# Kernel tuning notes

Hardware: AMD Instinct MI355X
Metric: run time of the kernel (lower is better)

Reference implementation:

```python
import jax, jax.numpy as jnp
import numpy as np

# Fixed architecture constants (from source / MambaConfig)
B_ = 8          # batch
L_ = 2048       # seq_len
D_MODEL = 6     # input_size / d_model
ED = 48         # expand_factor * d_model = hidden_size
N = 32          # d_state
DCONV = 16      # d_conv
NLAYERS = 4
DTRANK = 1      # ceil(d_model/16)
NCLASSES = 4
EPS = 1e-5


def setup_inputs() -> dict:
    key = jax.random.key(0)
    ks = jax.random.split(key, 10)
    def rn(k, shape, s=0.1):
        return jax.random.normal(k, shape, jnp.float32) * s
    return {
        "x": jax.random.normal(ks[0], (B_, L_, D_MODEL), jnp.float32),
        "in_proj_w": rn(ks[1], (NLAYERS, 2 * ED, D_MODEL)),
        "conv_w": rn(ks[2], (NLAYERS, ED, DCONV)),
        "conv_b": jnp.zeros((NLAYERS, ED), jnp.float32),
        "x_proj_w": rn(ks[3], (NLAYERS, DTRANK + 2 * N, ED)),
        "dt_proj_w": rn(ks[4], (NLAYERS, ED, DTRANK)),
        "dt_proj_b": rn(ks[5], (NLAYERS, ED), 0.05),
        "A_log": jnp.tile(jnp.log(jnp.arange(1, N + 1, dtype=jnp.float32)), (NLAYERS, ED, 1)),
        "D": jnp.ones((NLAYERS, ED), jnp.float32),
        "out_proj_w": rn(ks[6], (NLAYERS, D_MODEL, ED)),
        "norm_w": jnp.ones((NLAYERS, D_MODEL), jnp.float32),
        "fc_w": rn(ks[7], (NCLASSES, ED)),
        "fc_b": jnp.zeros((NCLASSES,), jnp.float32),
    }


def _dw_conv(x, w, b):
    # x: [B, L, ED], depthwise causal conv over L with kernel DCONV
    x_n = x.transpose(0, 2, 1)            # [B, ED, L]
    k = w[:, None, :]                      # [ED, 1, DCONV]
    y = jax.lax.conv_general_dilated(
        x_n, k, window_strides=(1,), padding=[(DCONV - 1, 0)],
        feature_group_count=ED, dimension_numbers=("NCH", "OIH", "NCH"))
    return (y + b[None, :, None]).transpose(0, 2, 1)  # [B, L, ED]


def _ssm(x_c, delta, A, Bm, Cm, Dp):
    # selective scan: h_t = exp(delta_t A) h_{t-1} + delta_t B_t x_t ; y_t = C_t . h_t + D x_t
    deltaA = jnp.exp(delta[..., None] * A)                    # [B,L,ED,N]
    deltaBx = (delta * x_c)[..., None] * Bm[:, :, None, :]    # [B,L,ED,N]
    def comb(c1, c2):
        a1, b1 = c1
        a2, b2 = c2
        return (a1 * a2, a2 * b1 + b2)
    _, h = jax.lax.associative_scan(comb, (deltaA, deltaBx), axis=1)
    y = jnp.einsum("blen,bln->ble", h, Cm) + Dp * x_c
    return y


def reference(x, in_proj_w, conv_w, conv_b, x_proj_w, dt_proj_w, dt_proj_b,
              A_log, D, out_proj_w, norm_w, fc_w, fc_b):
    h = x
    inner = None
    for i in range(NLAYERS):
        # RMSNorm (pre-norm)
        xn = h * jax.lax.rsqrt(jnp.mean(h * h, axis=-1, keepdims=True) + EPS) * norm_w[i]
        xz = xn @ in_proj_w[i].T                               # [B,L,2*ED]
        x_in, z = jnp.split(xz, 2, axis=-1)
        x_c = jax.nn.silu(_dw_conv(x_in, conv_w[i], conv_b[i]))
        dbl = x_c @ x_proj_w[i].T                              # [B,L,DTRANK+2N]
        dr = dbl[..., :DTRANK]
        Bm = dbl[..., DTRANK:DTRANK + N]
        Cm = dbl[..., DTRANK + N:]
        delta = jax.nn.softplus(dr @ dt_proj_w[i].T + dt_proj_b[i])  # [B,L,ED]
        A = -jnp.exp(A_log[i])                                 # [ED,N]
        y = _ssm(x_c, delta, A, Bm, Cm, D[i])
        y = y * jax.nn.silu(z)                                 # [B,L,ED]
        if i == NLAYERS - 1:
            inner = y  # classifier mode: keep 48-dim inner hidden
        else:
            h = y @ out_proj_w[i].T + h                        # residual in d_model
    last_hidden = inner[:, -1, :]                              # [B,ED]
    return last_hidden @ fc_w.T + fc_b                         # [B,NCLASSES]
```

## Files before the change

### kernel.cpp

```cpp
#include <hip/hip_runtime.h>
#include <math.h>

#define B_ 8
#define L_ 2048
#define DM 6
#define ED 48
#define NS 32
#define DCONV 16
#define NLAYERS 4
#define NCLASSES 4
#define EPS 1e-5f

#define CH 64
#define CL 32
#define HALO (DCONV - 1)
#define TP (CL + HALO)


__global__ void __launch_bounds__(256) k_fused_pre(
    const float* __restrict__ x,
    const float* __restrict__ yprev,
    const float* __restrict__ outw,
    const float* __restrict__ hin,
    float* __restrict__ hout,
    const float* __restrict__ ipw,
    const float* __restrict__ nw,
    const float* __restrict__ cw,
    const float* __restrict__ cb,
    const float* __restrict__ xpw,
    const float* __restrict__ dtw,
    const float* __restrict__ dtb,
    const float* __restrict__ A_log,
    float* __restrict__ z,
    float* __restrict__ xcg,
    float* __restrict__ delta,
    float* __restrict__ Bm, float* __restrict__ Cm,
    float* __restrict__ gA, float* __restrict__ gH,
    int layer)
{
    __shared__ float sh[DM][TP + 1];
    __shared__ float srn[TP + 1];
    __shared__ float sxin[ED][TP + 1];
    __shared__ float sxc[ED][CL + 1];
    __shared__ float sdel[ED][CL];
    __shared__ float sB[CL][NS + 1];
    __shared__ float sdr[CL];

    int b     = blockIdx.x >> 6;
    int chunk = blockIdx.x & (CH - 1);
    int l0    = chunk * CL;
    int tid   = threadIdx.x;

    for (int i = tid; i < DM * TP; i += 256) {
        int d = i / TP, p = i - d * TP;
        int l = l0 - HALO + p;
        float hv = 0.f;
        if (l >= 0) {
            if (layer == 0) {
                hv = x[((size_t)b * L_ + l) * DM + d];
            } else {
                hv = hin[((size_t)b * DM + d) * L_ + l];
                const float* yp = yprev + (size_t)b * ED * L_ + l;
                const float* wp = outw + d * ED;
                float acc = 0.f;
#pragma unroll
                for (int e = 0; e < ED; ++e) acc += yp[(size_t)e * L_] * wp[e];
                hv += acc;
            }
            if (p >= HALO && layer < NLAYERS - 1)
                hout[((size_t)b * DM + d) * L_ + l] = hv;
        }
        sh[d][p] = hv;
    }
    __syncthreads();

    if (tid < TP) {
        float ss = 0.f;
#pragma unroll
        for (int d = 0; d < DM; ++d) ss += sh[d][tid] * sh[d][tid];
        srn[tid] = rsqrtf(ss * (1.f / DM) + EPS);
    }
    __syncthreads();

    for (int i = tid; i < ED * TP; i += 256) {
        int e = i / TP, p = i - e * TP;
        const float* wp = ipw + e * DM;
        float acc = 0.f;
#pragma unroll
        for (int d = 0; d < DM; ++d) acc += sh[d][p] * nw[d] * wp[d];
        sxin[e][p] = acc * srn[p];
    }
    for (int i = tid; i < ED * CL; i += 256) {
        int e = i >> 5, po = i & 31;
        int p = po + HALO;
        const float* wp = ipw + (ED + e) * DM;
        float acc = 0.f;
#pragma unroll
        for (int d = 0; d < DM; ++d) acc += sh[d][p] * nw[d] * wp[d];
        z[((size_t)b * ED + e) * L_ + l0 + po] = acc * srn[p];
    }
    __syncthreads();

    for (int i = tid; i < ED * CL; i += 256) {
        int e = i >> 5, po = i & 31;
        const float* wp = cw + e * DCONV;
        float acc = cb[e];
#pragma unroll
        for (int k = 0; k < DCONV; ++k) acc += sxin[e][po + k] * wp[k];
        float v = acc / (1.f + __expf(-acc));
        sxc[e][po] = v;
        xcg[((size_t)b * ED + e) * L_ + l0 + po] = v;
    }
    __syncthreads();

    {
        int og = tid >> 5, li = tid & 31;
        int isB = og < 4;
        int nb = (og & 3) * 8;
        int rowBase = isB ? (1 + nb) : (1 + NS + nb);
        const float* wr = xpw + rowBase * ED;
        float a0=0,a1=0,a2=0,a3=0,a4=0,a5=0,a6=0,a7=0, dr=0;
#pragma unroll 4
        for (int e = 0; e < ED; ++e) {
            float xv = sxc[e][li];
            a0 += xv * wr[0*ED+e]; a1 += xv * wr[1*ED+e];
            a2 += xv * wr[2*ED+e]; a3 += xv * wr[3*ED+e];
            a4 += xv * wr[4*ED+e]; a5 += xv * wr[5*ED+e];
            a6 += xv * wr[6*ED+e]; a7 += xv * wr[7*ED+e];
            dr += xv * xpw[e];
        }
        float* outp = (isB ? Bm : Cm) + ((size_t)(b * L_ + l0 + li)) * NS + nb;
        ((float4*)outp)[0] = make_float4(a0, a1, a2, a3);
        ((float4*)outp)[1] = make_float4(a4, a5, a6, a7);
        if (isB) {
            float* dst = &sB[li][nb];
            dst[0]=a0; dst[1]=a1; dst[2]=a2; dst[3]=a3;
            dst[4]=a4; dst[5]=a5; dst[6]=a6; dst[7]=a7;
        }
        if (og == 0) sdr[li] = dr;
    }
    __syncthreads();

    for (int i = tid; i < ED * CL; i += 256) {
        int e = i >> 5, po = i & 31;
        float s = sdr[po] * dtw[e] + dtb[e];
        float dv = fmaxf(s, 0.f) + log1pf(__expf(-fabsf(s)));
        sdel[e][po] = dv;
        delta[((size_t)b * ED + e) * L_ + l0 + po] = dv;
    }
    __syncthreads();

    {
        int g2 = tid >> 5;
        int n  = tid & 31;
        int e0 = g2 * 6;
        float Aj[6], hb[6], sd[6];
#pragma unroll
        for (int j = 0; j < 6; ++j) {
            Aj[j] = -__expf(A_log[(e0 + j) * NS + n]);
            hb[j] = 0.f; sd[j] = 0.f;
        }
        for (int l = 0; l < CL; ++l) {
            float bb = sB[l][n];
#pragma unroll
            for (int j = 0; j < 6; ++j) {
                float dv = sdel[e0 + j][l];
                float xv = sxc[e0 + j][l];
                hb[j] = __expf(dv * Aj[j]) * hb[j] + (dv * xv) * bb;
                sd[j] += dv;
            }
        }
#pragma unroll
        for (int j = 0; j < 6; ++j) {
            size_t idx = ((size_t)(b * ED + e0 + j) * CH + chunk) * NS + n;
            gA[idx] = __expf(Aj[j] * sd[j]);
            gH[idx] = hb[j];
        }
    }
}

__global__ void __launch_bounds__(256) k_scan(
    const float* __restrict__ delta, const float* __restrict__ xc,
    const float* __restrict__ Bm, const float* __restrict__ Cm,
    const float* __restrict__ z,
    const float* __restrict__ A_log,
    const float* __restrict__ Dp,
    const float* __restrict__ gA, const float* __restrict__ gH,
    float* __restrict__ y,
    int lastLayer)
{
    int t = blockIdx.x * blockDim.x + threadIdx.x;
    int n = t & 31;
    int g = t >> 5;
    if (g >= B_ * ED * CH) return;
    int chunk = g & (CH - 1);
    int be    = g >> 6;
    if (lastLayer && chunk != CH - 1) return;
    int e = be % ED;
    int b = be / ED;
    float A  = -__expf(A_log[e * NS + n]);
    float Dv = Dp[e];

    float h = 0.f;
    {
        size_t base = (size_t)be * CH;
        for (int c = 0; c < chunk; ++c) {
            size_t idx = (base + c) * NS + n;
            h = gA[idx] * h + gH[idx];
        }
    }

    size_t eRow = (size_t)be * L_ + chunk * CL;
    size_t nRow = ((size_t)b * L_ + chunk * CL) * NS + n;
    const float4* dRow = (const float4*)(delta + eRow);
    const float4* xRow = (const float4*)(xc + eRow);
    const float* bBase = Bm + nRow;
    const float* cBase = Cm + nRow;
    const float* zRow  = z + eRow;
    float*       yRow  = y + eRow;
    int s0 = n & 1, s1 = n & 2;
    for (int q = 0; q < CL / 4; ++q) {
        float4 d4 = dRow[q];
        float4 x4 = xRow[q];
        float bb0 = bBase[(4 * q + 0) * NS];
        float bb1 = bBase[(4 * q + 1) * NS];
        float bb2 = bBase[(4 * q + 2) * NS];
        float bb3 = bBase[(4 * q + 3) * NS];
        float cc0 = cBase[(4 * q + 0) * NS];
        float cc1 = cBase[(4 * q + 1) * NS];
        float cc2 = cBase[(4 * q + 2) * NS];
        float cc3 = cBase[(4 * q + 3) * NS];
        h = __expf(d4.x*A)*h + (d4.x*x4.x)*bb0;  float p0 = h*cc0;
        h = __expf(d4.y*A)*h + (d4.y*x4.y)*bb1;  float p1 = h*cc1;
        h = __expf(d4.z*A)*h + (d4.z*x4.z)*bb2;  float p2 = h*cc2;
        h = __expf(d4.w*A)*h + (d4.w*x4.w)*bb3;  float p3 = h*cc3;
        float u  = s0 ? p1 : p0;
        float us = s0 ? p0 : p1;
        u += __shfl_xor(us, 1, 32);
        float v  = s0 ? p3 : p2;
        float vs = s0 ? p2 : p3;
        v += __shfl_xor(vs, 1, 32);
        float wv  = s1 ? v : u;
        float wvs = s1 ? u : v;
        wv += __shfl_xor(wvs, 2, 32);
        wv += __shfl_xor(wv, 4, 32);
        wv += __shfl_xor(wv, 8, 32);
        wv += __shfl_xor(wv, 16, 32);
        if (n < 4) {
            float xs = (n == 0) ? x4.x : (n == 1) ? x4.y
                     : (n == 2) ? x4.z : x4.w;
            float yr = wv + Dv * xs;
            float zv = zRow[4*q + n];
            yRow[4*q + n] = yr * (zv / (1.f + __expf(-zv)));
        }
    }
}

__global__ void k_cls(const float* __restrict__ y,
                      const float* __restrict__ fcw,
                      const float* __restrict__ fcb,
                      float* __restrict__ out)
{
    int t = threadIdx.x;
    if (t >= B_ * NCLASSES) return;
    int b = t / NCLASSES;
    int c = t - b * NCLASSES;
    const float* yp = y + (size_t)b * ED * L_ + (L_ - 1);
    const float* wp = fcw + c * ED;
    float acc = fcb[c];
#pragma unroll
    for (int e = 0; e < ED; ++e) acc += yp[(size_t)e * L_] * wp[e];
    out[t] = acc;
}

extern "C" void kernel_launch(void* const* d_in, const int* in_sizes, int n_in,
                              void* d_out, int out_size, void* d_ws, size_t ws_size,
                              hipStream_t stream)
{
    const float* x          = (const float*)d_in[0];
    const float* in_proj_w  = (const float*)d_in[1];
    const float* conv_w     = (const float*)d_in[2];
    const float* conv_b     = (const float*)d_in[3];
    const float* x_proj_w   = (const float*)d_in[4];
    const float* dt_proj_w  = (const float*)d_in[5];
    const float* dt_proj_b  = (const float*)d_in[6];
    const float* A_log      = (const float*)d_in[7];
    const float* Dp         = (const float*)d_in[8];
    const float* out_proj_w = (const float*)d_in[9];
    const float* norm_w     = (const float*)d_in[10];
    const float* fc_w       = (const float*)d_in[11];
    const float* fc_b       = (const float*)d_in[12];

    float* ws    = (float*)d_ws;
    float* z     = ws;
    float* xc    = z     + (size_t)B_ * ED * L_;
    float* delta = xc    + (size_t)B_ * ED * L_;
    float* y     = delta + (size_t)B_ * ED * L_;
    float* Bmat  = y     + (size_t)B_ * ED * L_;
    float* Cmat  = Bmat  + (size_t)B_ * L_ * NS;
    float* hA    = Cmat  + (size_t)B_ * L_ * NS;
    float* hB    = hA    + (size_t)B_ * DM * L_;
    float* gA    = hB    + (size_t)B_ * DM * L_;
    float* gH    = gA    + (size_t)B_ * ED * CH * NS;

    const int nScanT = B_ * ED * CH * NS;

    for (int i = 0; i < NLAYERS; ++i) {
        float* hout      = (i & 1) ? hB : hA;
        const float* hin = (i & 1) ? hA : hB;
        const float* ow  = (i == 0) ? out_proj_w
                                    : out_proj_w + (size_t)(i - 1) * DM * ED;
        k_fused_pre<<<B_ * CH, 256, 0, stream>>>(
            x, y, ow, hin, hout,
            in_proj_w + (size_t)i * 96 * DM, norm_w + (size_t)i * DM,
            conv_w + (size_t)i * ED * DCONV, conv_b + (size_t)i * ED,
            x_proj_w + (size_t)i * 65 * ED,
            dt_proj_w + (size_t)i * ED, dt_proj_b + (size_t)i * ED,
            A_log + (size_t)i * ED * NS,
            z, xc, delta, Bmat, Cmat, gA, gH, i);
        k_scan<<<(nScanT + 255) / 256, 256, 0, stream>>>(
            delta, xc, Bmat, Cmat, z,
            A_log + (size_t)i * ED * NS, Dp + (size_t)i * ED,
            gA, gH, y, (i == NLAYERS - 1) ? 1 : 0);
    }
    k_cls<<<1, 64, 0, stream>>>(y, fc_w, fc_b, (float*)d_out);
}
```

Before: 383.4 us.

## Restructure scan into per-(batch,chunk) blocks with shared-memory staging and fused classifier

The scan kernel is remapped so that each block handles one (batch, chunk) pair and covers all 48 channels, with each warp owning six channels. Delta, xc, z, B and C for the chunk are staged once into shared memory, so B and C are read from global memory once per block instead of once per channel. The classifier head is folded into the last-layer scan, which removes a separate kernel launch. The trade-off is far fewer blocks (512 instead of 12288), each warp running six serial recurrences with more register pressure, which lowers parallelism and latency hiding.

```diff
diff --git a/kernel.cpp b/kernel.cpp
--- a/kernel.cpp
+++ b/kernel.cpp
@@ -187,90 +187,115 @@
     const float* __restrict__ Dp,
     const float* __restrict__ gA, const float* __restrict__ gH,
     float* __restrict__ y,
+    const float* __restrict__ fcw, const float* __restrict__ fcb,
+    float* __restrict__ out,
     int lastLayer)
 {
-    int t = blockIdx.x * blockDim.x + threadIdx.x;
-    int n = t & 31;
-    int g = t >> 5;
-    if (g >= B_ * ED * CH) return;
-    int chunk = g & (CH - 1);
-    int be    = g >> 6;
+    __shared__ float sdel[ED][CL];
+    __shared__ float sxc[ED][CL];
+    __shared__ float sz[ED][CL];
+    __shared__ float sB[CL][NS];
+    __shared__ float sC[CL][NS];
+    __shared__ float sy[ED];
+
+    int b     = blockIdx.x >> 6;
+    int chunk = blockIdx.x & (CH - 1);
     if (lastLayer && chunk != CH - 1) return;
-    int e = be % ED;
-    int b = be / ED;
-    float A  = -__expf(A_log[e * NS + n]);
-    float Dv = Dp[e];
-
-    float h = 0.f;
+    int l0  = chunk * CL;
+    int tid = threadIdx.x;
+
+    for (int i = tid; i < ED * 8; i += 256) {
+        int e = i >> 3, q = i & 7;
+        size_t gi = ((size_t)(b * ED + e) * L_ + l0) / 4 + q;
+        ((float4*)sdel)[i] = ((const float4*)delta)[gi];
+        ((float4*)sxc)[i]  = ((const float4*)xc)[gi];
+        ((float4*)sz)[i]   = ((const float4*)z)[gi];
+    }
     {
-        size_t base = (size_t)be * CH;
-        for (int c = 0; c < chunk; ++c) {
-            size_t idx = (base + c) * NS + n;
-            h = gA[idx] * h + gH[idx];
-        }
-    }
-
-    size_t eRow = (size_t)be * L_ + chunk * CL;
-    size_t nRow = ((size_t)b * L_ + chunk * CL) * NS + n;
-    const float4* dRow = (const float4*)(delta + eRow);
-    const float4* xRow = (const float4*)(xc + eRow);
-    const float* bBase = Bm + nRow;
-    const float* cBase = Cm + nRow;
-    const float* zRow  = z + eRow;
-    float*       yRow  = y + eRow;
+        size_t gb = ((size_t)b * L_ + l0) * NS / 4;
+        ((float4*)sB)[tid] = ((const float4*)Bm)[gb + tid];
+        ((float4*)sC)[tid] = ((const float4*)Cm)[gb + tid];
+    }
+    __syncthreads();
+
+    int grp = tid >> 5;
+    int n   = tid & 31;
+    int e0  = grp * 6;
+
+    float Aj[6], h[6], Dv[6];
+#pragma unroll
+    for (int j = 0; j < 6; ++j) {
+        Aj[j] = -__expf(A_log[(e0 + j) * NS + n]);
+        Dv[j] = Dp[e0 + j];
+        h[j]  = 0.f;
+    }
+
+    for (int c = 0; c < chunk; ++c) {
+#pragma unroll
+        for (int j = 0; j < 6; ++j) {
+            size_t idx = ((size_t)(b * ED + e0 + j) * CH + c) * NS + n;
+            h[j] = gA[idx] * h[j] + gH[idx];
+        }
+    }
+
     int s0 = n & 1, s1 = n & 2;
+    const float4* sdel4 = (const float4*)sdel;
+    const float4* sxc4  = (const float4*)sxc;
+
     for (int q = 0; q < CL / 4; ++q) {
-        float4 d4 = dRow[q];
-        float4 x4 = xRow[q];
-        float bb0 = bBase[(4 * q + 0) * NS];
-        float bb1 = bBase[(4 * q + 1) * NS];
-        float bb2 = bBase[(4 * q + 2) * NS];
-        float bb3 = bBase[(4 * q + 3) * NS];
-        float cc0 = cBase[(4 * q + 0) * NS];
-        float cc1 = cBase[(4 * q + 1) * NS];
-        float cc2 = cBase[(4 * q + 2) * NS];
-        float cc3 = cBase[(4 * q + 3) * NS];
-        h = __expf(d4.x*A)*h + (d4.x*x4.x)*bb0;  float p0 = h*cc0;
-        h = __expf(d4.y*A)*h + (d4.y*x4.y)*bb1;  float p1 = h*cc1;
-        h = __expf(d4.z*A)*h + (d4.z*x4.z)*bb2;  float p2 = h*cc2;
-        h = __expf(d4.w*A)*h + (d4.w*x4.w)*bb3;  float p3 = h*cc3;
-        float u  = s0 ? p1 : p0;
-        float us = s0 ? p0 : p1;
-        u += __shfl_xor(us, 1, 32);
-        float v  = s0 ? p3 : p2;
-        float vs = s0 ? p2 : p3;
-        v += __shfl_xor(vs, 1, 32);
-        float wv  = s1 ? v : u;
-        float wvs = s1 ? u : v;
-        wv += __shfl_xor(wvs, 2, 32);
-        wv += __shfl_xor(wv, 4, 32);
-        wv += __shfl_xor(wv, 8, 32);
-        wv += __shfl_xor(wv, 16, 32);
-        if (n < 4) {
-            float xs = (n == 0) ? x4.x : (n == 1) ? x4.y
-                     : (n == 2) ? x4.z : x4.w;
-            float yr = wv + Dv * xs;
-            float zv = zRow[4*q + n];
-            yRow[4*q + n] = yr * (zv / (1.f + __expf(-zv)));
-        }
-    }
-}
-
-__global__ void k_cls(const float* __restrict__ y,
-                      const float* __restrict__ fcw,
-                      const float* __restrict__ fcb,
-                      float* __restrict__ out)
-{
-    int t = threadIdx.x;
-    if (t >= B_ * NCLASSES) return;
-    int b = t / NCLASSES;
-    int c = t - b * NCLASSES;
-    const float* yp = y + (size_t)b * ED * L_ + (L_ - 1);
-    const float* wp = fcw + c * ED;
-    float acc = fcb[c];
-#pragma unroll
-    for (int e = 0; e < ED; ++e) acc += yp[(size_t)e * L_] * wp[e];
-    out[t] = acc;
+        float bb0 = sB[4*q+0][n], bb1 = sB[4*q+1][n];
+        float bb2 = sB[4*q+2][n], bb3 = sB[4*q+3][n];
+        float cc0 = sC[4*q+0][n], cc1 = sC[4*q+1][n];
+        float cc2 = sC[4*q+2][n], cc3 = sC[4*q+3][n];
+        float p[6][4];
+        float4 xs[6];
+#pragma unroll
+        for (int j = 0; j < 6; ++j) {
+            float4 d4 = sdel4[(e0 + j) * 8 + q];
+            float4 x4 = sxc4[(e0 + j) * 8 + q];
+            xs[j] = x4;
+            float hj = h[j], A = Aj[j];
+            hj = __expf(d4.x*A)*hj + (d4.x*x4.x)*bb0;  p[j][0] = hj*cc0;
+            hj = __expf(d4.y*A)*hj + (d4.y*x4.y)*bb1;  p[j][1] = hj*cc1;
+            hj = __expf(d4.z*A)*hj + (d4.z*x4.z)*bb2;  p[j][2] = hj*cc2;
+            hj = __expf(d4.w*A)*hj + (d4.w*x4.w)*bb3;  p[j][3] = hj*cc3;
+            h[j] = hj;
+        }
+#pragma unroll
+        for (int j = 0; j < 6; ++j) {
+            float u  = s0 ? p[j][1] : p[j][0];
+            float us = s0 ? p[j][0] : p[j][1];
+            u += __shfl_xor(us, 1, 32);
+            float v  = s0 ? p[j][3] : p[j][2];
+            float vs = s0 ? p[j][2] : p[j][3];
+            v += __shfl_xor(vs, 1, 32);
+            float wv  = s1 ? v : u;
+            float wvs = s1 ? u : v;
+            wv += __shfl_xor(wvs, 2, 32);
+            wv += __shfl_xor(wv, 4, 32);
+            wv += __shfl_xor(wv, 8, 32);
+            wv += __shfl_xor(wv, 16, 32);
+            if (n < 4) {
+                float xv = (n == 0) ? xs[j].x : (n == 1) ? xs[j].y
+                         : (n == 2) ? xs[j].z : xs[j].w;
+                float yr = wv + Dv[j] * xv;
+                float zv = sz[e0 + j][4*q + n];
+                float yo = yr * (zv / (1.f + __expf(-zv)));
+                y[((size_t)(b * ED + e0 + j)) * L_ + l0 + 4*q + n] = yo;
+                if (lastLayer && q == CL/4 - 1 && n == 3) sy[e0 + j] = yo;
+            }
+        }
+    }
+
+    if (lastLayer) {
+        __syncthreads();
+        if (tid < NCLASSES) {
+            float acc = fcb[tid];
+#pragma unroll
+            for (int e = 0; e < ED; ++e) acc += sy[e] * fcw[tid * ED + e];
+            out[b * NCLASSES + tid] = acc;
+        }
+    }
 }
 
 extern "C" void kernel_launch(void* const* d_in, const int* in_sizes, int n_in,
@@ -303,8 +328,6 @@
     float* gA    = hB    + (size_t)B_ * DM * L_;
     float* gH    = gA    + (size_t)B_ * ED * CH * NS;
 
-    const int nScanT = B_ * ED * CH * NS;
-
     for (int i = 0; i < NLAYERS; ++i) {
         float* hout      = (i & 1) ? hB : hA;
         const float* hin = (i & 1) ? hA : hB;
@@ -318,10 +341,10 @@
             dt_proj_w + (size_t)i * ED, dt_proj_b + (size_t)i * ED,
             A_log + (size_t)i * ED * NS,
             z, xc, delta, Bmat, Cmat, gA, gH, i);
-        k_scan<<<(nScanT + 255) / 256, 256, 0, stream>>>(
+        k_scan<<<B_ * CH, 256, 0, stream>>>(
             delta, xc, Bmat, Cmat, z,
             A_log + (size_t)i * ED * NS, Dp + (size_t)i * ED,
-            gA, gH, y, (i == NLAYERS - 1) ? 1 : 0);
-    }
-    k_cls<<<1, 64, 0, stream>>>(y, fc_w, fc_b, (float*)d_out);
+            gA, gH, y, fc_w, fc_b, (float*)d_out,
+            (i == NLAYERS - 1) ? 1 : 0);
+    }
 }
```

Result: slower. 516.3 us (+34.7%).

## Fuse all Mamba layers into one cooperative persistent kernel with grid syncs

Applied to the files above, without the earlier changes.

Replaces the per-layer pair of kernels (fused pre-processing and chunked scan) plus the classifier kernel with a single cooperative kernel. Each block keeps its chunk's z, x_c, delta, B and C in shared memory, uses grid.sync between the chunk-summary pass and the scan, and again before the next layer reads the residual. The intra-chunk output is computed with shuffle reductions over the state dimension, and the out-projection and classifier are fused in. This removes the kernel launches and the global round trips for the intermediates, but depends on all 512 blocks being co-resident and adds grid-wide barriers. The old multi-kernel path is kept as a fallback if the cooperative launch fails.

```diff
diff --git a/kernel.cpp b/kernel.cpp
--- a/kernel.cpp
+++ b/kernel.cpp
@@ -1,5 +1,8 @@
 #include <hip/hip_runtime.h>
+#include <hip/hip_cooperative_groups.h>
 #include <math.h>
+
+namespace cg = cooperative_groups;
 
 #define B_ 8
 #define L_ 2048
@@ -16,23 +19,260 @@
 #define HALO (DCONV - 1)
 #define TP (CL + HALO)
 
+__global__ void __launch_bounds__(256, 2) k_mamba(
+    const float* __restrict__ x,
+    const float* __restrict__ in_proj_w,
+    const float* __restrict__ conv_w,
+    const float* __restrict__ conv_b,
+    const float* __restrict__ x_proj_w,
+    const float* __restrict__ dt_proj_w,
+    const float* __restrict__ dt_proj_b,
+    const float* __restrict__ A_log,
+    const float* __restrict__ Dp,
+    const float* __restrict__ out_proj_w,
+    const float* __restrict__ norm_w,
+    const float* __restrict__ fc_w,
+    const float* __restrict__ fc_b,
+    float* __restrict__ hA,
+    float* __restrict__ hB,
+    float* __restrict__ gA,
+    float* __restrict__ gH,
+    float* __restrict__ out)
+{
+    cg::grid_group grid = cg::this_grid();
+
+    __shared__ float sh[DM][TP + 1];
+    __shared__ float srn[TP + 1];
+    __shared__ float sxin[ED][TP + 1];
+    __shared__ float sxc[ED][CL];
+    __shared__ float sdel[ED][CL];
+    __shared__ float sz[ED][CL];
+    __shared__ float sB[CL][NS + 1];
+    __shared__ float sC[CL][NS + 1];
+    __shared__ float sdr[CL];
+    __shared__ float sy2d[ED][CL + 1];
+
+    int b     = blockIdx.x >> 6;
+    int chunk = blockIdx.x & (CH - 1);
+    int l0    = chunk * CL;
+    int tid   = threadIdx.x;
+    int grp   = tid >> 5;
+    int n     = tid & 31;
+    int e0    = grp * 6;
+
+    for (int layer = 0; layer < NLAYERS; ++layer) {
+        const float* ipw = in_proj_w + (size_t)layer * 2 * ED * DM;
+        const float* nw  = norm_w    + (size_t)layer * DM;
+        const float* cw  = conv_w    + (size_t)layer * ED * DCONV;
+        const float* cbp = conv_b    + (size_t)layer * ED;
+        const float* xpw = x_proj_w  + (size_t)layer * (1 + 2 * NS) * ED;
+        const float* dtw = dt_proj_w + (size_t)layer * ED;
+        const float* dtb = dt_proj_b + (size_t)layer * ED;
+        const float* Alg = A_log     + (size_t)layer * ED * NS;
+        const float* Dpl = Dp        + (size_t)layer * ED;
+        const float* hin = (layer & 1) ? hA : hB;
+        float*       hout= (layer & 1) ? hB : hA;
+
+        for (int i = tid; i < DM * TP; i += 256) {
+            int d = i / TP, p = i - d * TP;
+            int l = l0 - HALO + p;
+            float hv = 0.f;
+            if (l >= 0)
+                hv = (layer == 0) ? x[((size_t)b * L_ + l) * DM + d]
+                                  : hin[((size_t)b * DM + d) * L_ + l];
+            sh[d][p] = hv;
+        }
+        __syncthreads();
+
+        if (tid < TP) {
+            float ss = 0.f;
+#pragma unroll
+            for (int d = 0; d < DM; ++d) ss += sh[d][tid] * sh[d][tid];
+            srn[tid] = rsqrtf(ss * (1.f / DM) + EPS);
+        }
+        __syncthreads();
+
+        for (int i = tid; i < ED * TP; i += 256) {
+            int e = i / TP, p = i - e * TP;
+            const float* wp = ipw + e * DM;
+            float acc = 0.f;
+#pragma unroll
+            for (int d = 0; d < DM; ++d) acc += sh[d][p] * nw[d] * wp[d];
+            sxin[e][p] = acc * srn[p];
+        }
+        for (int i = tid; i < ED * CL; i += 256) {
+            int e = i >> 5, po = i & 31;
+            int p = po + HALO;
+            const float* wp = ipw + (ED + e) * DM;
+            float acc = 0.f;
+#pragma unroll
+            for (int d = 0; d < DM; ++d) acc += sh[d][p] * nw[d] * wp[d];
+            sz[e][po] = acc * srn[p];
+        }
+        __syncthreads();
+
+        for (int i = tid; i < ED * CL; i += 256) {
+            int e = i >> 5, po = i & 31;
+            const float* wp = cw + e * DCONV;
+            float acc = cbp[e];
+#pragma unroll
+            for (int k = 0; k < DCONV; ++k) acc += sxin[e][po + k] * wp[k];
+            sxc[e][po] = acc / (1.f + __expf(-acc));
+        }
+        __syncthreads();
+
+        {
+            int isB = grp < 4;
+            int nb  = (grp & 3) * 8;
+            int rowBase = isB ? (1 + nb) : (1 + NS + nb);
+            const float* wr = xpw + rowBase * ED;
+            float a0=0,a1=0,a2=0,a3=0,a4=0,a5=0,a6=0,a7=0, dr=0;
+#pragma unroll 4
+            for (int e = 0; e < ED; ++e) {
+                float xv = sxc[e][n];
+                a0 += xv * wr[0*ED+e]; a1 += xv * wr[1*ED+e];
+                a2 += xv * wr[2*ED+e]; a3 += xv * wr[3*ED+e];
+                a4 += xv * wr[4*ED+e]; a5 += xv * wr[5*ED+e];
+                a6 += xv * wr[6*ED+e]; a7 += xv * wr[7*ED+e];
+                dr += xv * xpw[e];
+            }
+            float* dst = isB ? &sB[n][nb] : &sC[n][nb];
+            dst[0]=a0; dst[1]=a1; dst[2]=a2; dst[3]=a3;
+            dst[4]=a4; dst[5]=a5; dst[6]=a6; dst[7]=a7;
+            if (grp == 0) sdr[n] = dr;
+        }
+        __syncthreads();
+
+        for (int i = tid; i < ED * CL; i += 256) {
+            int e = i >> 5, po = i & 31;
+            float s = sdr[po] * dtw[e] + dtb[e];
+            sdel[e][po] = fmaxf(s, 0.f) + log1pf(__expf(-fabsf(s)));
+        }
+        __syncthreads();
+
+        float Aj[6];
+        {
+            float hb[6], sd[6];
+#pragma unroll
+            for (int j = 0; j < 6; ++j) {
+                Aj[j] = -__expf(Alg[(e0 + j) * NS + n]);
+                hb[j] = 0.f; sd[j] = 0.f;
+            }
+            for (int l = 0; l < CL; ++l) {
+                float bb = sB[l][n];
+#pragma unroll
+                for (int j = 0; j < 6; ++j) {
+                    float dv = sdel[e0 + j][l];
+                    float xv = sxc[e0 + j][l];
+                    hb[j] = __expf(dv * Aj[j]) * hb[j] + (dv * xv) * bb;
+                    sd[j] += dv;
+                }
+            }
+#pragma unroll
+            for (int j = 0; j < 6; ++j) {
+                size_t idx = ((size_t)(b * ED + e0 + j) * CH + chunk) * NS + n;
+                gA[idx] = __expf(Aj[j] * sd[j]);
+                gH[idx] = hb[j];
+            }
+        }
+        __threadfence();
+        grid.sync();
+
+        bool active = (layer < NLAYERS - 1) || (chunk == CH - 1);
+        if (active) {
+            float h[6], Dv[6];
+#pragma unroll
+            for (int j = 0; j < 6; ++j) { h[j] = 0.f; Dv[j] = Dpl[e0 + j]; }
+            for (int c = 0; c < chunk; ++c) {
+#pragma unroll
+                for (int j = 0; j < 6; ++j) {
+                    size_t idx = ((size_t)(b * ED + e0 + j) * CH + c) * NS + n;
+                    h[j] = gA[idx] * h[j] + gH[idx];
+                }
+            }
+            int s0 = n & 1, s1 = n & 2;
+            const float4* sdel4 = (const float4*)sdel;
+            const float4* sxc4  = (const float4*)sxc;
+            for (int q = 0; q < CL / 4; ++q) {
+                float bb0 = sB[4*q+0][n], bb1 = sB[4*q+1][n];
+                float bb2 = sB[4*q+2][n], bb3 = sB[4*q+3][n];
+                float cc0 = sC[4*q+0][n], cc1 = sC[4*q+1][n];
+                float cc2 = sC[4*q+2][n], cc3 = sC[4*q+3][n];
+                float p[6][4];
+                float4 xs[6];
+#pragma unroll
+                for (int j = 0; j < 6; ++j) {
+                    float4 d4 = sdel4[(e0 + j) * (CL/4) + q];
+                    float4 x4 = sxc4[(e0 + j) * (CL/4) + q];
+                    xs[j] = x4;
+                    float hj = h[j], A = Aj[j];
+                    hj = __expf(d4.x*A)*hj + (d4.x*x4.x)*bb0;  p[j][0] = hj*cc0;
+                    hj = __expf(d4.y*A)*hj + (d4.y*x4.y)*bb1;  p[j][1] = hj*cc1;
+                    hj = __expf(d4.z*A)*hj + (d4.z*x4.z)*bb2;  p[j][2] = hj*cc2;
+                    hj = __expf(d4.w*A)*hj + (d4.w*x4.w)*bb3;  p[j][3] = hj*cc3;
+                    h[j] = hj;
+                }
+#pragma unroll
+                for (int j = 0; j < 6; ++j) {
+                    float u  = s0 ? p[j][1] : p[j][0];
+                    float us = s0 ? p[j][0] : p[j][1];
+                    u += __shfl_xor(us, 1, 32);
+                    float v  = s0 ? p[j][3] : p[j][2];
+                    float vs = s0 ? p[j][2] : p[j][3];
+                    v += __shfl_xor(vs, 1, 32);
+                    float wv  = s1 ? v : u;
+                    float wvs = s1 ? u : v;
+                    wv += __shfl_xor(wvs, 2, 32);
+                    wv += __shfl_xor(wv, 4, 32);
+                    wv += __shfl_xor(wv, 8, 32);
+                    wv += __shfl_xor(wv, 16, 32);
+                    if (n < 4) {
+                        float xv = (n == 0) ? xs[j].x : (n == 1) ? xs[j].y
+                                 : (n == 2) ? xs[j].z : xs[j].w;
+                        float yr = wv + Dv[j] * xv;
+                        float zv = sz[e0 + j][4*q + n];
+                        sy2d[e0 + j][4*q + n] = yr * (zv / (1.f + __expf(-zv)));
+                    }
+                }
+            }
+        }
+
+        if (layer < NLAYERS - 1) {
+            __syncthreads();
+            const float* ow = out_proj_w + (size_t)layer * DM * ED;
+            for (int i = tid; i < DM * CL; i += 256) {
+                int d = i >> 5, po = i & 31;
+                const float* wp = ow + d * ED;
+                float acc = sh[d][po + HALO];
+#pragma unroll
+                for (int e = 0; e < ED; ++e) acc += sy2d[e][po] * wp[e];
+                hout[((size_t)b * DM + d) * L_ + l0 + po] = acc;
+            }
+            __threadfence();
+            grid.sync();
+        } else if (chunk == CH - 1) {
+            __syncthreads();
+            if (tid < NCLASSES) {
+                float acc = fc_b[tid];
+#pragma unroll
+                for (int e = 0; e < ED; ++e)
+                    acc += sy2d[e][CL - 1] * fc_w[tid * ED + e];
+                out[b * NCLASSES + tid] = acc;
+            }
+        }
+    }
+}
 
 __global__ void __launch_bounds__(256) k_fused_pre(
-    const float* __restrict__ x,
-    const float* __restrict__ yprev,
-    const float* __restrict__ outw,
-    const float* __restrict__ hin,
+    const float* __restrict__ x, const float* __restrict__ yprev,
+    const float* __restrict__ outw, const float* __restrict__ hin,
     float* __restrict__ hout,
-    const float* __restrict__ ipw,
-    const float* __restrict__ nw,
-    const float* __restrict__ cw,
-    const float* __restrict__ cb,
+    const float* __restrict__ ipw, const float* __restrict__ nw,
+    const float* __restrict__ cw, const float* __restrict__ cb,
     const float* __restrict__ xpw,
-    const float* __restrict__ dtw,
-    const float* __restrict__ dtb,
+    const float* __restrict__ dtw, const float* __restrict__ dtb,
     const float* __restrict__ A_log,
-    float* __restrict__ z,
-    float* __restrict__ xcg,
+    float* __restrict__ z, float* __restrict__ xcg,
     float* __restrict__ delta,
     float* __restrict__ Bm, float* __restrict__ Cm,
     float* __restrict__ gA, float* __restrict__ gH,
@@ -183,11 +423,9 @@
     const float* __restrict__ delta, const float* __restrict__ xc,
     const float* __restrict__ Bm, const float* __restrict__ Cm,
     const float* __restrict__ z,
-    const float* __restrict__ A_log,
-    const float* __restrict__ Dp,
+    const float* __restrict__ A_log, const float* __restrict__ Dp,
     const float* __restrict__ gA, const float* __restrict__ gH,
-    float* __restrict__ y,
-    int lastLayer)
+    float* __restrict__ y, int lastLayer)
 {
     int t = blockIdx.x * blockDim.x + threadIdx.x;
     int n = t & 31;
@@ -302,9 +540,21 @@
     float* hB    = hA    + (size_t)B_ * DM * L_;
     float* gA    = hB    + (size_t)B_ * DM * L_;
     float* gH    = gA    + (size_t)B_ * ED * CH * NS;
+    float* outp  = (float*)d_out;
+
+    void* args[] = {
+        (void*)&x, (void*)&in_proj_w, (void*)&conv_w, (void*)&conv_b,
+        (void*)&x_proj_w, (void*)&dt_proj_w, (void*)&dt_proj_b,
+        (void*)&A_log, (void*)&Dp, (void*)&out_proj_w, (void*)&norm_w,
+        (void*)&fc_w, (void*)&fc_b,
+        (void*)&hA, (void*)&hB, (void*)&gA, (void*)&gH, (void*)&outp
+    };
+    hipError_t err = hipLaunchCooperativeKernel(
+        reinterpret_cast<void*>(k_mamba),
+        dim3(B_ * CH), dim3(256), args, 0, stream);
+    if (err == hipSuccess) return;
 
     const int nScanT = B_ * ED * CH * NS;
-
     for (int i = 0; i < NLAYERS; ++i) {
         float* hout      = (i & 1) ? hB : hA;
         const float* hin = (i & 1) ? hA : hB;
@@ -323,5 +573,5 @@
             A_log + (size_t)i * ED * NS, Dp + (size_t)i * ED,
             gA, gH, y, (i == NLAYERS - 1) ? 1 : 0);
     }
-    k_cls<<<1, 64, 0, stream>>>(y, fc_w, fc_b, (float*)d_out);
+    k_cls<<<1, 64, 0, stream>>>(y, fc_w, fc_b, outp);
 }
```

Result: slower. 1.090 ms (+184.2%).
